# Kernel tuning notes

Hardware: AMD Instinct MI355X
Metric: run time of the kernel (lower is better)

The kernel has to match this reference:

```python
import jax, jax.numpy as jnp
import numpy as np

C = 1.0
SQRT_C = 1.0
EPS = 4e-3        # Poincare ball proj eps for float32
MIN_NORM = 1e-15
N_NODES = 50000
N_EDGES = 800000
NFEAT, NOUT, NHID, HEADS = 128, 64, 32, 4


def _norm(t):
    return jnp.clip(jnp.linalg.norm(t, axis=-1, keepdims=True), MIN_NORM)


def artanh(t):
    t = jnp.clip(t, -1.0 + 1e-7, 1.0 - 1e-7)
    return 0.5 * (jnp.log1p(t) - jnp.log1p(-t))


def proj(t):
    n = _norm(t)
    maxnorm = (1.0 - EPS) / SQRT_C
    return jnp.where(n > maxnorm, t / n * maxnorm, t)


def expmap0(u):
    n = _norm(u)
    return jnp.tanh(SQRT_C * n) * u / (SQRT_C * n)


def logmap0(p):
    n = _norm(p)
    return artanh(SQRT_C * n) * p / (SQRT_C * n)


def mobius_add(a, b):
    a2 = jnp.sum(a * a, -1, keepdims=True)
    b2 = jnp.sum(b * b, -1, keepdims=True)
    ab = jnp.sum(a * b, -1, keepdims=True)
    num = (1.0 + 2.0 * C * ab + C * b2) * a + (1.0 - C * a2) * b
    den = 1.0 + 2.0 * C * ab + C * C * a2 * b2
    return num / jnp.clip(den, MIN_NORM)


def mobius_matvec(W, t):
    mx = t @ W.T
    xn = _norm(t)
    mxn = _norm(mx)
    res = jnp.tanh(mxn / xn * artanh(SQRT_C * xn)) * mx / (mxn * SQRT_C)
    zero = jnp.all(mx == 0, axis=-1, keepdims=True)
    return jnp.where(zero, jnp.zeros_like(res), res)


def hyp_linear(t, W, b):
    res = proj(mobius_matvec(W, t))
    hyp_b = proj(expmap0(b[None, :]))  # proj_tan0 is identity on Poincare ball
    return proj(mobius_add(res, hyp_b))


def leaky_relu(t, slope):
    return jnp.where(t >= 0, t, slope * t)


def hyp_att_agg(h, src, dst, att_i, att_j, heads, concat):
    n = h.shape[0]
    d = h.shape[1] // heads
    ht = logmap0(h)                          # tangent space at origin
    x_i = ht[src].reshape(-1, heads, d)      # target (aggregation) endpoint
    x_j = ht[dst].reshape(-1, heads, d)      # source (message) endpoint
    alpha = (x_i * att_i).sum(-1) + (x_j * att_j).sum(-1)   # [E, heads]
    alpha = leaky_relu(alpha, 0.2)
    amax = jax.ops.segment_max(alpha, src, num_segments=n)
    e = jnp.exp(alpha - amax[src])
    denom = jax.ops.segment_sum(e, src, num_segments=n)
    alpha = e / (denom[src] + 1e-16)
    out = jax.ops.segment_sum(x_j * alpha[..., None], src, num_segments=n)  # [N,h,d]
    out = out.reshape(n, heads * d) if concat else out.mean(axis=1)
    return proj(expmap0(out))


def hyp_act(h, slope=0.01):
    return proj(expmap0(leaky_relu(logmap0(h), slope)))


def _glorot(key, shape):
    fan = shape[-1] + (shape[-2] if len(shape) > 1 else shape[-1])
    a = np.sqrt(6.0 / fan).astype(np.float32)
    return jax.random.uniform(key, shape, jnp.float32, -a, a)


def setup_inputs() -> dict:
    key = jax.random.key(0)
    ks = jax.random.split(key, 12)
    return {
        "x": jax.random.normal(ks[0], (N_NODES, NFEAT), jnp.float32),
        "Wl": _glorot(ks[1], (NOUT, NFEAT)),
        "bl": jnp.zeros((NOUT,), jnp.float32),
        "W1": _glorot(ks[2], (NHID * HEADS, NOUT)),
        "b1": jnp.zeros((NHID * HEADS,), jnp.float32),
        "ai1": _glorot(ks[3], (1, HEADS, NHID)),
        "aj1": _glorot(ks[4], (1, HEADS, NHID)),
        "W2": _glorot(ks[5], (NOUT * HEADS, NHID * HEADS)),
        "b2": jnp.zeros((NOUT * HEADS,), jnp.float32),
        "ai2": _glorot(ks[6], (1, HEADS, NOUT)),
        "aj2": _glorot(ks[7], (1, HEADS, NOUT)),
        "edge_index": jax.random.randint(ks[8], (2, N_EDGES), 0, N_NODES, jnp.int64 if jax.config.jax_enable_x64 else jnp.int32),
    }


def reference(x, Wl, bl, W1, b1, ai1, aj1, W2, b2, ai2, aj2, edge_index):
    n = x.shape[0]
    loops = jnp.arange(n, dtype=edge_index.dtype)
    ei = jnp.concatenate([edge_index, jnp.stack([loops, loops])], axis=1)
    src, dst = ei[0], ei[1]
    h = x @ Wl.T + bl                     # Euclidean linear
    h = proj(expmap0(h))                  # initHyperX (proj_tan0 = identity)
    h = proj(h)
    # layer1: HGATConv(nout -> nhid, heads, concat=True)
    h = hyp_linear(h, W1, b1)
    h = hyp_att_agg(h, src, dst, ai1, aj1, HEADS, True)
    h = hyp_act(h)
    h = proj(h)
    # layer2: HGATConv(nhid*heads -> nout, heads, concat=False)
    h = hyp_linear(h, W2, b2)
    h = hyp_att_agg(h, src, dst, ai2, aj2, HEADS, False)
    h = hyp_act(h)
    return logmap0(h)                     # toTangentX (proj_tan0 = identity)
```

## Files before the change

### kernel.cpp

```cpp
#include <hip/hip_runtime.h>
#include <hip/hip_fp16.h>

#define NN 50000
#define NER 800000
#define NE 850000
#define MAXN 0.996f
#define MINNRM 1e-15f
#define SCAN_B 256
#define NBLK ((NN + SCAN_B - 1) / SCAN_B)
#define HB ((NE + 255) / 256)
#define G0B ((NN + 63) / 64)

typedef _Float16 h2 __attribute__((ext_vector_type(2)));
union UB4 { uint4 u; h2 h[4]; };

__device__ __forceinline__ h2 f2h2(float a, float b){ h2 r; r.x=(_Float16)a; r.y=(_Float16)b; return r; }
__device__ __forceinline__ h2 splat(float a){ h2 r; r.x=(_Float16)a; r.y=(_Float16)a; return r; }

__device__ __forceinline__ float gsum16(float v){
  v += __shfl_xor(v, 1, 64); v += __shfl_xor(v, 2, 64);
  v += __shfl_xor(v, 4, 64); v += __shfl_xor(v, 8, 64);
  return v;
}
__device__ __forceinline__ float gmax16(float v){
  v = fmaxf(v, __shfl_xor(v, 1, 64)); v = fmaxf(v, __shfl_xor(v, 2, 64));
  v = fmaxf(v, __shfl_xor(v, 4, 64)); v = fmaxf(v, __shfl_xor(v, 8, 64));
  return v;
}
__device__ __forceinline__ float artanh_c(float t){
  t = fminf(t, 1.0f - 1e-7f);
  return 0.5f * (log1pf(t) - log1pf(-t));
}
__device__ __forceinline__ float lrelu(float t, float s){ return t >= 0.f ? t : s * t; }

__device__ void bias_blk(const float* b, const float* ai, const float* aj, int L, int HS, float* hbx){
  __shared__ float red[256];
  __shared__ float hai[4], haj[4];
  int t = threadIdx.x;
  float v = (t < L) ? b[t] : 0.f;
  red[t] = v * v; __syncthreads();
  for (int s = 128; s; s >>= 1){ if (t < s) red[t] += red[t + s]; __syncthreads(); }
  float n  = fmaxf(sqrtf(red[0]), MINNRM);
  float un = tanhf(n);
  float nn = un;
  float f  = un / n;
  if (un > MAXN){ f = MAXN / n; nn = MAXN; }
  float hb = v * f;
  if (t < L) hbx[t] = hb;
  if (t < 4){ hai[t] = 0.f; haj[t] = 0.f; }
  __syncthreads();
  if (t < L){
    int h = t / HS;
    atomicAdd(&hai[h], hb * ai[t]);
    atomicAdd(&haj[h], hb * aj[t]);
  }
  __syncthreads();
  if (t == 0) hbx[L] = nn * nn;
  if (t < 4){ hbx[L + 1 + t] = hai[t]; hbx[L + 5 + t] = haj[t]; }
}

__device__ __forceinline__ void wconv(const float* in, __half* outp, int Nr, int Kc, int i){
  int tot = Nr * (Kc >> 1);
  if (i >= tot) return;
  int kp = i / Nr, n = i % Nr;
  __half2 v;
  v.x = __float2half(in[(size_t)n * Kc + 2 * kp]);
  v.y = __float2half(in[(size_t)n * Kc + 2 * kp + 1]);
  ((__half2*)outp)[i] = v;
}

__global__ __launch_bounds__(256) void kprep(
    const float* __restrict__ b1, const float* __restrict__ ai1, const float* __restrict__ aj1, float* __restrict__ hbx1,
    const float* __restrict__ b2, const float* __restrict__ ai2, const float* __restrict__ aj2, float* __restrict__ hbx2,
    const float* __restrict__ Wl, __half* __restrict__ Wlh,
    const float* __restrict__ W1, __half* __restrict__ W1h,
    const float* __restrict__ W2, __half* __restrict__ W2h,
    const int* __restrict__ ei, int* __restrict__ cnt, int* __restrict__ rank){
  int bid = blockIdx.x, tid = threadIdx.x;
  if (bid == 0){ bias_blk(b1, ai1, aj1, 128, 32, hbx1); return; }
  if (bid == 1){ bias_blk(b2, ai2, aj2, 256, 64, hbx2); return; }
  if (bid < 18){ wconv(Wl, Wlh, 64, 128, (bid - 2) * 256 + tid); return; }
  if (bid < 34){ wconv(W1, W1h, 128, 64, (bid - 18) * 256 + tid); return; }
  if (bid < 98){ wconv(W2, W2h, 256, 128, (bid - 34) * 256 + tid); return; }
  int e = (bid - 98) * 256 + tid;
  if (e >= NE) return;
  int s = (e < NER) ? ei[e] : (e - NER);
  rank[e] = atomicAdd(&cnt[s], 1);
}

__device__ void kg0_body(int bid, const float* __restrict__ x, const __half* __restrict__ Wlh,
                         const float* __restrict__ bl, __half* __restrict__ h0h,
                         float* __restrict__ xn0){
  __shared__ __align__(16) h2 As2[16][68];
  __shared__ __align__(16) h2 Bs2[16][68];
  __shared__ float red[64][2];
  int tid = threadIdx.x, wave = tid >> 6, lane = tid & 63;
  int wr = wave >> 1, wc = wave & 1, lr = lane >> 3, lc = lane & 7;
  int row0 = bid * 64;
  int r0 = wr * 32 + lr * 4, c0 = wc * 32 + lc * 4;
  float acc[4][4] = {};
  int am = tid >> 2, aq = tid & 3;
  int bkp = tid >> 4, bn4 = (tid & 15) * 4;
  const uint* Wlu = (const uint*)Wlh;
  float4 ra0, ra1; uint4 rb;
  {
    int row = row0 + am;
    ra0 = make_float4(0.f,0.f,0.f,0.f); ra1 = ra0;
    if (row < NN){
      ra0 = *(const float4*)(x + (size_t)row * 128 + aq * 8);
      ra1 = *(const float4*)(x + (size_t)row * 128 + aq * 8 + 4);
    }
    rb = *(const uint4*)(Wlu + (size_t)bkp * 64 + bn4);
  }
  for (int ks = 0; ks < 4; ks++){
    __syncthreads();
    As2[aq*4+0][am] = f2h2(ra0.x, ra0.y);
    As2[aq*4+1][am] = f2h2(ra0.z, ra0.w);
    As2[aq*4+2][am] = f2h2(ra1.x, ra1.y);
    As2[aq*4+3][am] = f2h2(ra1.z, ra1.w);
    *(uint4*)&Bs2[bkp][bn4] = rb;
    __syncthreads();
    if (ks < 3){
      int k0 = (ks + 1) * 32;
      int row = row0 + am;
      ra0 = make_float4(0.f,0.f,0.f,0.f); ra1 = ra0;
      if (row < NN){
        ra0 = *(const float4*)(x + (size_t)row * 128 + k0 + aq * 8);
        ra1 = *(const float4*)(x + (size_t)row * 128 + k0 + aq * 8 + 4);
      }
      rb = *(const uint4*)(Wlu + (size_t)((ks + 1) * 16 + bkp) * 64 + bn4);
    }
#pragma unroll
    for (int kp = 0; kp < 16; kp++){
      UB4 av, bv;
      av.u = *(const uint4*)&As2[kp][r0];
      bv.u = *(const uint4*)&Bs2[kp][c0];
#pragma unroll
      for (int i = 0; i < 4; i++)
#pragma unroll
        for (int j = 0; j < 4; j++)
          acc[i][j] = __builtin_amdgcn_fdot2(av.h[i], bv.h[j], acc[i][j], false);
    }
  }
  float bb[4];
  *(float4*)&bb[0] = *(const float4*)(bl + c0);
#pragma unroll
  for (int i = 0; i < 4; i++){
    float rs = 0.f;
#pragma unroll
    for (int j = 0; j < 4; j++){ acc[i][j] += bb[j]; rs = fmaf(acc[i][j], acc[i][j], rs); }
    rs += __shfl_xor(rs, 1, 64);
    rs += __shfl_xor(rs, 2, 64);
    rs += __shfl_xor(rs, 4, 64);
    if (lc == 0) red[r0 + i][wc] = rs;
  }
  __syncthreads();
#pragma unroll
  for (int i = 0; i < 4; i++){
    int row = row0 + r0 + i;
    if (row >= NN) continue;
    float rs = red[r0 + i][0] + red[r0 + i][1];
    float n  = fmaxf(sqrtf(rs), MINNRM);
    float un = tanhf(n);
    float f, nm;
    if (un > MAXN){ f = MAXN / n; nm = MAXN; } else { f = un / n; nm = un; }
    union { uint2 u; __half2 h[2]; } st;
    st.h[0] = __floats2half2_rn(acc[i][0] * f, acc[i][1] * f);
    st.h[1] = __floats2half2_rn(acc[i][2] * f, acc[i][3] * f);
    *(uint2*)(h0h + (size_t)row * 64 + c0) = st.u;
    if (wc == 0 && lc == 0) xn0[row] = nm;
  }
}

__global__ __launch_bounds__(256) void kB(const int* __restrict__ cnt,
                                          int* __restrict__ part, int* __restrict__ bsum,
                                          const float* __restrict__ x, const __half* __restrict__ Wlh,
                                          const float* __restrict__ bl, __half* __restrict__ h0h,
                                          float* __restrict__ xn0){
  int bid = blockIdx.x;
  if (bid < NBLK){
    __shared__ int sh[SCAN_B];
    int t = threadIdx.x;
    int i = bid * SCAN_B + t;
    int v = (i < NN) ? cnt[i] : 0;
    sh[t] = v; __syncthreads();
    for (int d = 1; d < SCAN_B; d <<= 1){
      int u = (t >= d) ? sh[t - d] : 0;
      __syncthreads();
      sh[t] += u;
      __syncthreads();
    }
    if (i < NN) part[i] = sh[t];
    if (t == SCAN_B - 1) bsum[bid] = sh[t];
    return;
  }
  kg0_body(bid - NBLK, x, Wlh, bl, h0h, xn0);
}

__global__ __launch_bounds__(256) void kscan2(int* __restrict__ bsum){
  __shared__ int sh[256];
  int t = threadIdx.x;
  int v = (t < NBLK) ? bsum[t] : 0;
  sh[t] = v; __syncthreads();
  for (int d = 1; d < 256; d <<= 1){
    int u = (t >= d) ? sh[t - d] : 0;
    __syncthreads();
    sh[t] += u;
    __syncthreads();
  }
  if (t < NBLK) bsum[t] = sh[t];
}

__global__ __launch_bounds__(SCAN_B) void kscan3(const int* __restrict__ part, const int* __restrict__ bsum,
                                                 const int* __restrict__ cnt, int* __restrict__ rowptr){
  int t = threadIdx.x;
  int i = blockIdx.x * SCAN_B + t;
  if (i < NN){
    int base = blockIdx.x ? bsum[blockIdx.x - 1] : 0;
    rowptr[i] = base + part[i] - cnt[i];
  }
  if (i == 0) rowptr[NN] = bsum[NBLK - 1];
}

__device__ void kg1f_body(int bid, const __half* __restrict__ Ah, const __half* __restrict__ W1h,
    const float* __restrict__ xn0, const float* __restrict__ hbx,
    const float* __restrict__ ai, const float* __restrict__ aj,
    __half* __restrict__ ht1, float* __restrict__ s1i, float* __restrict__ s1j){
  __shared__ __align__(16) h2 As2[16][68];
  __shared__ __align__(16) h2 Bs2[16][132];
  __shared__ float red[64][12];
  int tid = threadIdx.x, wave = tid >> 6, lane = tid & 63;
  int wr = wave >> 1, wc = wave & 1, lr = lane >> 3, lc = lane & 7;
  int row0 = bid * 64;
  int r0 = wr * 32 + lr * 4, c0 = wc * 64 + lc * 8;
  float acc[4][8] = {};
  const uint* Au = (const uint*)Ah;
  const uint* Bu = (const uint*)W1h;
  int akp = tid & 15, am0 = (tid >> 4) * 4;
  int bkp = tid >> 4, bcol = (tid & 15) * 4;
  uint ua0, ua1, ua2, ua3; uint4 ub0, ub1;
  {
    int r;
    ua0 = ua1 = ua2 = ua3 = 0u;
    r = row0 + am0 + 0; if (r < NN) ua0 = Au[(size_t)r * 32 + akp];
    r = row0 + am0 + 1; if (r < NN) ua1 = Au[(size_t)r * 32 + akp];
    r = row0 + am0 + 2; if (r < NN) ua2 = Au[(size_t)r * 32 + akp];
    r = row0 + am0 + 3; if (r < NN) ua3 = Au[(size_t)r * 32 + akp];
    ub0 = *(const uint4*)(Bu + (size_t)bkp * 128 + bcol);
    ub1 = *(const uint4*)(Bu + (size_t)bkp * 128 + bcol + 64);
  }
  for (int ks = 0; ks < 2; ks++){
    __syncthreads();
    { uint4 av4; av4.x = ua0; av4.y = ua1; av4.z = ua2; av4.w = ua3;
      *(uint4*)&As2[akp][am0] = av4; }
    *(uint4*)&Bs2[bkp][bcol]      = ub0;
    *(uint4*)&Bs2[bkp][bcol + 64] = ub1;
    __syncthreads();
    if (ks < 1){
      int r;
      ua0 = ua1 = ua2 = ua3 = 0u;
      r = row0 + am0 + 0; if (r < NN) ua0 = Au[(size_t)r * 32 + 16 + akp];
      r = row0 + am0 + 1; if (r < NN) ua1 = Au[(size_t)r * 32 + 16 + akp];
      r = row0 + am0 + 2; if (r < NN) ua2 = Au[(size_t)r * 32 + 16 + akp];
      r = row0 + am0 + 3; if (r < NN) ua3 = Au[(size_t)r * 32 + 16 + akp];
      ub0 = *(const uint4*)(Bu + (size_t)(16 + bkp) * 128 + bcol);
      ub1 = *(const uint4*)(Bu + (size_t)(16 + bkp) * 128 + bcol + 64);
    }
#pragma unroll
    for (int kp = 0; kp < 16; kp++){
      UB4 av, bv0, bv1;
      av.u  = *(const uint4*)&As2[kp][r0];
      bv0.u = *(const uint4*)&Bs2[kp][c0];
      bv1.u = *(const uint4*)&Bs2[kp][c0 + 4];
#pragma unroll
      for (int i = 0; i < 4; i++){
#pragma unroll
        for (int j = 0; j < 4; j++)
          acc[i][j] = __builtin_amdgcn_fdot2(av.h[i], bv0.h[j], acc[i][j], false);
#pragma unroll
        for (int j = 4; j < 8; j++)
          acc[i][j] = __builtin_amdgcn_fdot2(av.h[i], bv1.h[j - 4], acc[i][j], false);
      }
    }
  }
  float hbv[8], aiv[8], ajv[8];
  *(float4*)&hbv[0] = *(const float4*)(hbx + c0); *(float4*)&hbv[4] = *(const float4*)(hbx + c0 + 4);
  *(float4*)&aiv[0] = *(const float4*)(ai + c0);  *(float4*)&aiv[4] = *(const float4*)(ai + c0 + 4);
  *(float4*)&ajv[0] = *(const float4*)(aj + c0);  *(float4*)&ajv[4] = *(const float4*)(aj + c0 + 4);
  float b2 = hbx[128];
  int head = wc * 2 + (lc >> 2);
#pragma unroll
  for (int i = 0; i < 4; i++){
    float p1=0.f, p2=0.f, pai=0.f, paj=0.f;
#pragma unroll
    for (int j = 0; j < 8; j++){
      float a = acc[i][j];
      p1 += a*a; p2 += a*hbv[j]; pai += a*aiv[j]; paj += a*ajv[j];
    }
    p1 += __shfl_xor(p1,1,64); p1 += __shfl_xor(p1,2,64); p1 += __shfl_xor(p1,4,64);
    p2 += __shfl_xor(p2,1,64); p2 += __shfl_xor(p2,2,64); p2 += __shfl_xor(p2,4,64);
    pai += __shfl_xor(pai,1,64); pai += __shfl_xor(pai,2,64);
    paj += __shfl_xor(paj,1,64); paj += __shfl_xor(paj,2,64);
    int rloc = r0 + i;
    if (lc == 0){ red[rloc][wc] = p1; red[rloc][2+wc] = p2; }
    if ((lc & 3) == 0){ red[rloc][4+head] = pai; red[rloc][8+head] = paj; }
  }
  __syncthreads();
#pragma unroll
  for (int i = 0; i < 4; i++){
    int row = row0 + r0 + i;
    if (row >= NN) continue;
    int rloc = r0 + i;
    float S1 = red[rloc][0] + red[rloc][1];
    float S2 = red[rloc][2] + red[rloc][3];
    float xn = fmaxf(xn0[row], MINNRM);
    float r_art = artanh_c(xn);
    float mxn = fmaxf(sqrtf(S1), MINNRM);
    float tn = tanhf(mxn / xn * r_art);
    float sc_ = tn / mxn;
    float rn = tn;
    if (rn > MAXN){ sc_ *= MAXN / rn; rn = MAXN; }
    float a2r = rn * rn;
    float ab = sc_ * S2;
    float co1 = 1.f + 2.f*ab + b2, co2 = 1.f - a2r;
    float den = fmaxf(1.f + 2.f*ab + a2r*b2, MINNRM);
    float P = co1 * sc_ / den, Q = co2 / den;
    float hn2 = P*P*S1 + 2.f*P*Q*S2 + Q*Q*b2;
    float hn = fmaxf(sqrtf(hn2), MINNRM);
    if (hn > MAXN){ float R = MAXN / hn; P *= R; Q *= R; hn = MAXN; }
    float lf = artanh_c(hn) / hn;
    union { __half h[8]; float4 f4; } ho;
#pragma unroll
    for (int j = 0; j < 8; j++) ho.h[j] = __float2half(lf * (P * acc[i][j] + Q * hbv[j]));
    *(float4*)(ht1 + (size_t)row * 128 + c0) = ho.f4;
    if (lc == 0){
      float pi0 = lf * (P * red[rloc][4+2*wc]   + Q * hbx[129+2*wc]);
      float pi1 = lf * (P * red[rloc][4+2*wc+1] + Q * hbx[129+2*wc+1]);
      float pj0 = lf * (P * red[rloc][8+2*wc]   + Q * hbx[133+2*wc]);
      float pj1 = lf * (P * red[rloc][8+2*wc+1] + Q * hbx[133+2*wc+1]);
      s1i[row*4+2*wc] = pi0; s1i[row*4+2*wc+1] = pi1;
      s1j[row*4+2*wc] = pj0; s1j[row*4+2*wc+1] = pj1;
    }
  }
}

__global__ __launch_bounds__(256) void kE(const int* __restrict__ ei, const int* __restrict__ rowptr,
    const int* __restrict__ rank, int* __restrict__ col,
    const __half* __restrict__ Ah, const __half* __restrict__ W1h,
    const float* __restrict__ xn0, const float* __restrict__ hbx,
    const float* __restrict__ ai, const float* __restrict__ aj,
    __half* __restrict__ ht1, float* __restrict__ s1i, float* __restrict__ s1j){
  int bid = blockIdx.x;
  if (bid >= G0B){
    int e = (bid - G0B) * 256 + threadIdx.x;
    if (e >= NE) return;
    int s, d;
    if (e < NER){ s = ei[e]; d = ei[NER + e]; }
    else { s = e - NER; d = s; }
    col[rowptr[s] + rank[e]] = d;
    return;
  }
  kg1f_body(bid, Ah, W1h, xn0, hbx, ai, aj, ht1, s1i, s1j);
}

__global__ __launch_bounds__(256) void kg2f(const __half* __restrict__ Ah, const __half* __restrict__ W2h,
    const float* __restrict__ xn1, const float* __restrict__ hbx,
    const float* __restrict__ ai, const float* __restrict__ aj,
    __half* __restrict__ ht2, float* __restrict__ s2i, float* __restrict__ s2j){
  __shared__ __align__(16) h2 As2[16][36];
  __shared__ __align__(16) h2 Bs2[16][260];
  __shared__ float red[32][16];
  int tid = threadIdx.x, wave = tid >> 6, lane = tid & 63;
  int wc = wave, lr = lane >> 3, lc = lane & 7;
  int row0 = blockIdx.x * 32;
  int r0 = lr * 4, c0 = wc * 64 + lc * 8;
  float acc[4][8] = {};
  const uint* Au = (const uint*)Ah;
  const uint* Bu = (const uint*)W2h;
  int akp = tid & 15, am0 = (tid >> 4) * 2;
  int brow = tid >> 4, bcol = (tid & 15) * 4;
  uint ua0, ua1;
  uint4 ub0, ub1, ub2, ub3;
  {
    int r;
    ua0 = ua1 = 0u;
    r = row0 + am0 + 0; if (r < NN) ua0 = Au[(size_t)r * 64 + akp];
    r = row0 + am0 + 1; if (r < NN) ua1 = Au[(size_t)r * 64 + akp];
    ub0 = *(const uint4*)(Bu + (size_t)brow * 256 + bcol);
    ub1 = *(const uint4*)(Bu + (size_t)brow * 256 + bcol + 64);
    ub2 = *(const uint4*)(Bu + (size_t)brow * 256 + bcol + 128);
    ub3 = *(const uint4*)(Bu + (size_t)brow * 256 + bcol + 192);
  }
  for (int ks = 0; ks < 4; ks++){
    __syncthreads();
    { uint2 av2; av2.x = ua0; av2.y = ua1;
      *(uint2*)&As2[akp][am0] = av2; }
    *(uint4*)&Bs2[brow][bcol]       = ub0;
    *(uint4*)&Bs2[brow][bcol + 64]  = ub1;
    *(uint4*)&Bs2[brow][bcol + 128] = ub2;
    *(uint4*)&Bs2[brow][bcol + 192] = ub3;
    __syncthreads();
    if (ks < 3){
      int kq = (ks + 1) * 16;
      int r;
      ua0 = ua1 = 0u;
      r = row0 + am0 + 0; if (r < NN) ua0 = Au[(size_t)r * 64 + kq + akp];
      r = row0 + am0 + 1; if (r < NN) ua1 = Au[(size_t)r * 64 + kq + akp];
      ub0 = *(const uint4*)(Bu + (size_t)(kq + brow) * 256 + bcol);
      ub1 = *(const uint4*)(Bu + (size_t)(kq + brow) * 256 + bcol + 64);
      ub2 = *(const uint4*)(Bu + (size_t)(kq + brow) * 256 + bcol + 128);
      ub3 = *(const uint4*)(Bu + (size_t)(kq + brow) * 256 + bcol + 192);
    }
#pragma unroll
    for (int kp = 0; kp < 16; kp++){
      UB4 av, bv0, bv1;
      av.u  = *(const uint4*)&As2[kp][r0];
      bv0.u = *(const uint4*)&Bs2[kp][c0];
      bv1.u = *(const uint4*)&Bs2[kp][c0 + 4];
#pragma unroll
      for (int i = 0; i < 4; i++){
#pragma unroll
        for (int j = 0; j < 4; j++)
          acc[i][j] = __builtin_amdgcn_fdot2(av.h[i], bv0.h[j], acc[i][j], false);
#pragma unroll
        for (int j = 4; j < 8; j++)
          acc[i][j] = __builtin_amdgcn_fdot2(av.h[i], bv1.h[j - 4], acc[i][j], false);
      }
    }
  }
  float hbv[8], aiv[8], ajv[8];
  *(float4*)&hbv[0] = *(const float4*)(hbx + c0); *(float4*)&hbv[4] = *(const float4*)(hbx + c0 + 4);
  *(float4*)&aiv[0] = *(const float4*)(ai + c0);  *(float4*)&aiv[4] = *(const float4*)(ai + c0 + 4);
  *(float4*)&ajv[0] = *(const float4*)(aj + c0);  *(float4*)&ajv[4] = *(const float4*)(aj + c0 + 4);
  float b2 = hbx[256];
#pragma unroll
  for (int i = 0; i < 4; i++){
    float p1=0.f, p2=0.f, pai=0.f, paj=0.f;
#pragma unroll
    for (int j = 0; j < 8; j++){
      float a = acc[i][j];
      p1 += a*a; p2 += a*hbv[j]; pai += a*aiv[j]; paj += a*ajv[j];
    }
    p1 += __shfl_xor(p1,1,64); p1 += __shfl_xor(p1,2,64); p1 += __shfl_xor(p1,4,64);
    p2 += __shfl_xor(p2,1,64); p2 += __shfl_xor(p2,2,64); p2 += __shfl_xor(p2,4,64);
    pai += __shfl_xor(pai,1,64); pai += __shfl_xor(pai,2,64); pai += __shfl_xor(pai,4,64);
    paj += __shfl_xor(paj,1,64); paj += __shfl_xor(paj,2,64); paj += __shfl_xor(paj,4,64);
    int rloc = r0 + i;
    if (lc == 0){ red[rloc][wc] = p1; red[rloc][4+wc] = p2; red[rloc][8+wc] = pai; red[rloc][12+wc] = paj; }
  }
  __syncthreads();
#pragma unroll
  for (int i = 0; i < 4; i++){
    int row = row0 + r0 + i;
    if (row >= NN) continue;
    int rloc = r0 + i;
    float S1 = red[rloc][0]+red[rloc][1]+red[rloc][2]+red[rloc][3];
    float S2 = red[rloc][4]+red[rloc][5]+red[rloc][6]+red[rloc][7];
    float xn = fmaxf(xn1[row], MINNRM);
    float r_art = artanh_c(xn);
    float mxn = fmaxf(sqrtf(S1), MINNRM);
    float tn = tanhf(mxn / xn * r_art);
    float sc_ = tn / mxn;
    float rn = tn;
    if (rn > MAXN){ sc_ *= MAXN / rn; rn = MAXN; }
    float a2r = rn * rn;
    float ab = sc_ * S2;
    float co1 = 1.f + 2.f*ab + b2, co2 = 1.f - a2r;
    float den = fmaxf(1.f + 2.f*ab + a2r*b2, MINNRM);
    float P = co1 * sc_ / den, Q = co2 / den;
    float hn2 = P*P*S1 + 2.f*P*Q*S2 + Q*Q*b2;
    float hn = fmaxf(sqrtf(hn2), MINNRM);
    if (hn > MAXN){ float R = MAXN / hn; P *= R; Q *= R; hn = MAXN; }
    float lf = artanh_c(hn) / hn;
    union { __half h[8]; float4 f4; } ho;
#pragma unroll
    for (int j = 0; j < 8; j++) ho.h[j] = __float2half(lf * (P * acc[i][j] + Q * hbv[j]));
    *(float4*)(ht2 + (size_t)row * 256 + c0) = ho.f4;
    if (lc == 0){
      float pi = lf * (P * red[rloc][8+wc]  + Q * hbx[257+wc]);
      float pj = lf * (P * red[rloc][12+wc] + Q * hbx[261+wc]);
      s2i[row*4+wc] = pi; s2j[row*4+wc] = pj;
    }
  }
}

__global__ __launch_bounds__(256) void k_agg1(const int* __restrict__ rowptr, const int* __restrict__ col,
    const __half* __restrict__ ht1, const float* __restrict__ s1i, const float* __restrict__ s1j,
    __half* __restrict__ hacth, float* __restrict__ xn1){
  __shared__ int    sd[4][4][68];
  __shared__ float4 swl[4][4][66];
  int tid = threadIdx.x, wave = tid >> 6, lane = tid & 63;
  int g = lane >> 4, l = lane & 15, hh = l >> 2;
  int n = blockIdx.x * 16 + wave * 4 + g;
  int p0 = rowptr[n], p1 = rowptr[n + 1];
  float4 si = *(const float4*)(s1i + (size_t)n * 4);
  float m0=-1e30f,m1=-1e30f,m2=-1e30f,m3=-1e30f;
  float s0=0.f,s1=0.f,s2=0.f,s3=0.f;
  h2 acc2[4] = {};
  for (int base = p0; base < p1; base += 64){
    float a[4][4];
#pragma unroll
    for (int ss = 0; ss < 4; ss++){
      a[ss][0] = a[ss][1] = a[ss][2] = a[ss][3] = -1e30f;
      int e = base + ss * 16 + l;
      if (e < p1){
        int d = col[e];
        float4 sj = *(const float4*)(s1j + (size_t)d * 4);
        a[ss][0] = lrelu(si.x + sj.x, 0.2f);
        a[ss][1] = lrelu(si.y + sj.y, 0.2f);
        a[ss][2] = lrelu(si.z + sj.z, 0.2f);
        a[ss][3] = lrelu(si.w + sj.w, 0.2f);
        sd[wave][g][ss * 16 + l] = d;
      }
    }
    float c0 = fmaxf(fmaxf(a[0][0], a[1][0]), fmaxf(a[2][0], a[3][0]));
    float c1 = fmaxf(fmaxf(a[0][1], a[1][1]), fmaxf(a[2][1], a[3][1]));
    float c2 = fmaxf(fmaxf(a[0][2], a[1][2]), fmaxf(a[2][2], a[3][2]));
    float c3 = fmaxf(fmaxf(a[0][3], a[1][3]), fmaxf(a[2][3], a[3][3]));
    float nm0 = fmaxf(m0, gmax16(c0)), nm1 = fmaxf(m1, gmax16(c1));
    float nm2 = fmaxf(m2, gmax16(c2)), nm3 = fmaxf(m3, gmax16(c3));
    float r0_ = __expf(m0 - nm0), r1_ = __expf(m1 - nm1);
    float r2_ = __expf(m2 - nm2), r3_ = __expf(m3 - nm3);
    float t0 = 0.f, t1 = 0.f, t2 = 0.f, t3 = 0.f;
#pragma unroll
    for (int ss = 0; ss < 4; ss++){
      float w0 = __expf(a[ss][0] - nm0), w1 = __expf(a[ss][1] - nm1);
      float w2 = __expf(a[ss][2] - nm2), w3 = __expf(a[ss][3] - nm3);
      swl[wave][g][ss * 16 + l] = make_float4(w0, w1, w2, w3);
      t0 += w0; t1 += w1; t2 += w2; t3 += w3;
    }
    s0 = s0 * r0_ + gsum16(t0); s1 = s1 * r1_ + gsum16(t1);
    s2 = s2 * r2_ + gsum16(t2); s3 = s3 * r3_ + gsum16(t3);
    m0 = nm0; m1 = nm1; m2 = nm2; m3 = nm3;
    float rsel = (hh==0)?r0_:(hh==1)?r1_:(hh==2)?r2_:r3_;
    h2 rs2 = splat(rsel);
#pragma unroll
    for (int j = 0; j < 4; j++) acc2[j] = acc2[j] * rs2;
    __builtin_amdgcn_wave_barrier();
    int cnt_ = min(p1 - base, 64);
    int e = 0;
    for (; e + 3 < cnt_; e += 4){
      int dA = sd[wave][g][e],   dB = sd[wave][g][e+1];
      int dC = sd[wave][g][e+2], dD = sd[wave][g][e+3];
      h2 wA2 = splat(((const float*)&swl[wave][g][e])[hh]);
      h2 wB2 = splat(((const float*)&swl[wave][g][e+1])[hh]);
      h2 wC2 = splat(((const float*)&swl[wave][g][e+2])[hh]);
      h2 wD2 = splat(((const float*)&swl[wave][g][e+3])[hh]);
      UB4 uA, uB, uC, uD;
      uA.u = *(const uint4*)(ht1 + (size_t)dA * 128 + 8*l);
      uB.u = *(const uint4*)(ht1 + (size_t)dB * 128 + 8*l);
      uC.u = *(const uint4*)(ht1 + (size_t)dC * 128 + 8*l);
      uD.u = *(const uint4*)(ht1 + (size_t)dD * 128 + 8*l);
#pragma unroll
      for (int j = 0; j < 4; j++){
        acc2[j] = acc2[j] + wA2 * uA.h[j] + wB2 * uB.h[j] + wC2 * uC.h[j] + wD2 * uD.h[j];
      }
    }
    for (; e < cnt_; e++){
      int dA = sd[wave][g][e];
      h2 wA2 = splat(((const float*)&swl[wave][g][e])[hh]);
      UB4 uA;
      uA.u = *(const uint4*)(ht1 + (size_t)dA * 128 + 8*l);
#pragma unroll
      for (int j = 0; j < 4; j++) acc2[j] = acc2[j] + wA2 * uA.h[j];
    }
    __builtin_amdgcn_wave_barrier();
  }
  float ssel = (hh==0)?s0:(hh==1)?s1:(hh==2)?s2:s3;
  float rinv = 1.f / (ssel + 1e-16f);
  float accf[8];
#pragma unroll
  for (int j = 0; j < 4; j++){ accf[2*j] = (float)acc2[j].x; accf[2*j+1] = (float)acc2[j].y; }
  float sum2 = 0.f;
#pragma unroll
  for (int j = 0; j < 8; j++){ accf[j] *= rinv; sum2 = fmaf(accf[j], accf[j], sum2); }
  sum2 = gsum16(sum2);
  float nn = fmaxf(sqrtf(sum2), MINNRM);
  float un = tanhf(nn);
  float f_, uN;
  if (un > MAXN){ f_ = MAXN / nn; uN = MAXN; } else { f_ = un / nn; uN = un; }
  float lg = artanh_c(uN) / fmaxf(uN, MINNRM);
  float tt[8]; float sum2b = 0.f;
#pragma unroll
  for (int j = 0; j < 8; j++){ tt[j] = lrelu(accf[j] * f_ * lg, 0.01f); sum2b = fmaf(tt[j], tt[j], sum2b); }
  sum2b = gsum16(sum2b);
  float nn2 = fmaxf(sqrtf(sum2b), MINNRM);
  float un2 = tanhf(nn2);
  float f2, nm2v;
  if (un2 > MAXN){ f2 = MAXN / nn2; nm2v = MAXN; } else { f2 = un2 / nn2; nm2v = un2; }
  union { uint4 u; __half2 h[4]; } st;
  st.h[0] = __floats2half2_rn(tt[0]*f2, tt[1]*f2);
  st.h[1] = __floats2half2_rn(tt[2]*f2, tt[3]*f2);
  st.h[2] = __floats2half2_rn(tt[4]*f2, tt[5]*f2);
  st.h[3] = __floats2half2_rn(tt[6]*f2, tt[7]*f2);
  *(uint4*)(hacth + (size_t)n * 128 + 8*l) = st.u;
  if (l == 0) xn1[n] = nm2v;
}

__global__ __launch_bounds__(256) void k_agg2(const int* __restrict__ rowptr, const int* __restrict__ col,
    const __half* __restrict__ ht2, const float* __restrict__ s2i, const float* __restrict__ s2j,
    float* __restrict__ out){
  __shared__ int    sd[4][4][68];
  __shared__ float4 swl[4][4][66];
  int tid = threadIdx.x, wave = tid >> 6, lane = tid & 63;
  int g = lane >> 4, l = lane & 15, hh = l >> 2;
  int n = blockIdx.x * 16 + wave * 4 + g;
  int p0 = rowptr[n], p1 = rowptr[n + 1];
  float4 si = *(const float4*)(s2i + (size_t)n * 4);
  float m0=-1e30f,m1=-1e30f,m2=-1e30f,m3=-1e30f;
  float s0=0.f,s1=0.f,s2=0.f,s3=0.f;
  h2 acc2[8] = {};
  for (int base = p0; base < p1; base += 64){
    float a[4][4];
#pragma unroll
    for (int ss = 0; ss < 4; ss++){
      a[ss][0] = a[ss][1] = a[ss][2] = a[ss][3] = -1e30f;
      int e = base + ss * 16 + l;
      if (e < p1){
        int d = col[e];
        float4 sj = *(const float4*)(s2j + (size_t)d * 4);
        a[ss][0] = lrelu(si.x + sj.x, 0.2f);
        a[ss][1] = lrelu(si.y + sj.y, 0.2f);
        a[ss][2] = lrelu(si.z + sj.z, 0.2f);
        a[ss][3] = lrelu(si.w + sj.w, 0.2f);
        sd[wave][g][ss * 16 + l] = d;
      }
    }
    float c0 = fmaxf(fmaxf(a[0][0], a[1][0]), fmaxf(a[2][0], a[3][0]));
    float c1 = fmaxf(fmaxf(a[0][1], a[1][1]), fmaxf(a[2][1], a[3][1]));
    float c2 = fmaxf(fmaxf(a[0][2], a[1][2]), fmaxf(a[2][2], a[3][2]));
    float c3 = fmaxf(fmaxf(a[0][3], a[1][3]), fmaxf(a[2][3], a[3][3]));
    float nm0 = fmaxf(m0, gmax16(c0)), nm1 = fmaxf(m1, gmax16(c1));
    float nm2 = fmaxf(m2, gmax16(c2)), nm3 = fmaxf(m3, gmax16(c3));
    float r0_ = __expf(m0 - nm0), r1_ = __expf(m1 - nm1);
    float r2_ = __expf(m2 - nm2), r3_ = __expf(m3 - nm3);
    float t0 = 0.f, t1 = 0.f, t2 = 0.f, t3 = 0.f;
#pragma unroll
    for (int ss = 0; ss < 4; ss++){
      float w0 = __expf(a[ss][0] - nm0), w1 = __expf(a[ss][1] - nm1);
      float w2 = __expf(a[ss][2] - nm2), w3 = __expf(a[ss][3] - nm3);
      swl[wave][g][ss * 16 + l] = make_float4(w0, w1, w2, w3);
      t0 += w0; t1 += w1; t2 += w2; t3 += w3;
    }
    s0 = s0 * r0_ + gsum16(t0); s1 = s1 * r1_ + gsum16(t1);
    s2 = s2 * r2_ + gsum16(t2); s3 = s3 * r3_ + gsum16(t3);
    m0 = nm0; m1 = nm1; m2 = nm2; m3 = nm3;
    float rsel = (hh==0)?r0_:(hh==1)?r1_:(hh==2)?r2_:r3_;
    h2 rs2 = splat(rsel);
#pragma unroll
    for (int j = 0; j < 8; j++) acc2[j] = acc2[j] * rs2;
    __builtin_amdgcn_wave_barrier();
    int cnt_ = min(p1 - base, 64);
    int e = 0;
    for (; e + 3 < cnt_; e += 4){
      int dA = sd[wave][g][e],   dB = sd[wave][g][e+1];
      int dC = sd[wave][g][e+2], dD = sd[wave][g][e+3];
      h2 wA2 = splat(((const float*)&swl[wave][g][e])[hh]);
      h2 wB2 = splat(((const float*)&swl[wave][g][e+1])[hh]);
      h2 wC2 = splat(((const float*)&swl[wave][g][e+2])[hh]);
      h2 wD2 = splat(((const float*)&swl[wave][g][e+3])[hh]);
      const __half* pA = ht2 + (size_t)dA * 256 + 16*l;
      const __half* pB = ht2 + (size_t)dB * 256 + 16*l;
      const __half* pC = ht2 + (size_t)dC * 256 + 16*l;
      const __half* pD = ht2 + (size_t)dD * 256 + 16*l;
      UB4 uA0, uA1, uB0, uB1, uC0, uC1, uD0, uD1;
      uA0.u = *(const uint4*)pA; uA1.u = *(const uint4*)(pA + 8);
      uB0.u = *(const uint4*)pB; uB1.u = *(const uint4*)(pB + 8);
      uC0.u = *(const uint4*)pC; uC1.u = *(const uint4*)(pC + 8);
      uD0.u = *(const uint4*)pD; uD1.u = *(const uint4*)(pD + 8);
#pragma unroll
      for (int j = 0; j < 4; j++){
        acc2[j]   = acc2[j]   + wA2 * uA0.h[j] + wB2 * uB0.h[j] + wC2 * uC0.h[j] + wD2 * uD0.h[j];
        acc2[4+j] = acc2[4+j] + wA2 * uA1.h[j] + wB2 * uB1.h[j] + wC2 * uC1.h[j] + wD2 * uD1.h[j];
      }
    }
    for (; e < cnt_; e++){
      int dA = sd[wave][g][e];
      h2 wA2 = splat(((const float*)&swl[wave][g][e])[hh]);
      const __half* pA = ht2 + (size_t)dA * 256 + 16*l;
      UB4 uA0, uA1;
      uA0.u = *(const uint4*)pA; uA1.u = *(const uint4*)(pA + 8);
#pragma unroll
      for (int j = 0; j < 4; j++){
        acc2[j]   = acc2[j]   + wA2 * uA0.h[j];
        acc2[4+j] = acc2[4+j] + wA2 * uA1.h[j];
      }
    }
    __builtin_amdgcn_wave_barrier();
  }
  float ssel = (hh==0)?s0:(hh==1)?s1:(hh==2)?s2:s3;
  float rinv = 1.f / (ssel + 1e-16f);
  float accf[16];
#pragma unroll
  for (int j = 0; j < 4; j++){
    accf[2*j]     = (float)acc2[j].x;   accf[2*j+1]   = (float)acc2[j].y;
    accf[8+2*j]   = (float)acc2[4+j].x; accf[8+2*j+1] = (float)acc2[4+j].y;
  }
  float mj[16]; float sum2 = 0.f;
#pragma unroll
  for (int j = 0; j < 16; j++){
    float v = accf[j] * rinv;
    v += __shfl_xor(v, 4, 64);
    v += __shfl_xor(v, 8, 64);
    mj[j] = 0.25f * v;
    sum2 = fmaf(mj[j], mj[j], sum2);
  }
  sum2 = 0.25f * gsum16(sum2);
  float nn = fmaxf(sqrtf(sum2), MINNRM);
  float un = tanhf(nn);
  float f_, uN;
  if (un > MAXN){ f_ = MAXN / nn; uN = MAXN; } else { f_ = un / nn; uN = un; }
  float lg = artanh_c(uN) / fmaxf(uN, MINNRM);
  float tt[16]; float sum2b = 0.f;
#pragma unroll
  for (int j = 0; j < 16; j++){ tt[j] = lrelu(mj[j] * f_ * lg, 0.01f); sum2b = fmaf(tt[j], tt[j], sum2b); }
  sum2b = 0.25f * gsum16(sum2b);
  float nn2 = fmaxf(sqrtf(sum2b), MINNRM);
  float un2 = tanhf(nn2);
  float f2 = (un2 > MAXN) ? (MAXN / nn2) : (un2 / nn2);
  float uN2 = fminf(un2, MAXN);
  float lg2 = artanh_c(uN2) / fmaxf(uN2, MINNRM);
  if (hh == 0){
    float o[16];
#pragma unroll
    for (int j = 0; j < 16; j++) o[j] = tt[j] * f2 * lg2;
    float* op = out + (size_t)n * 64 + 16*l;
    *(float4*)op      = *(float4*)&o[0];
    *(float4*)(op+4)  = *(float4*)&o[4];
    *(float4*)(op+8)  = *(float4*)&o[8];
    *(float4*)(op+12) = *(float4*)&o[12];
  }
}

extern "C" void kernel_launch(void* const* d_in, const int* in_sizes, int n_in,
                              void* d_out, int out_size, void* d_ws, size_t ws_size,
                              hipStream_t stream){
  const float* x   = (const float*)d_in[0];
  const float* Wl  = (const float*)d_in[1];
  const float* bl  = (const float*)d_in[2];
  const float* W1  = (const float*)d_in[3];
  const float* b1  = (const float*)d_in[4];
  const float* ai1 = (const float*)d_in[5];
  const float* aj1 = (const float*)d_in[6];
  const float* W2  = (const float*)d_in[7];
  const float* b2  = (const float*)d_in[8];
  const float* ai2 = (const float*)d_in[9];
  const float* aj2 = (const float*)d_in[10];
  const int*   ei  = (const int*)d_in[11];
  float* out = (float*)d_out;
  float* ws  = (float*)d_ws;

  __half* h0h   = (__half*)(ws);
  __half* ht1h  = (__half*)(ws + 1600000);
  __half* hacth = (__half*)(ws + 4800000);
  __half* ht2h  = (__half*)(ws + 8000000);
  float* xn0    = ws + 14400000;
  float* xn1    = ws + 14450000;
  float* s1i    = ws + 14500000;
  float* s1j    = ws + 14700000;
  float* hbx1   = ws + 14900000;
  float* hbx2   = ws + 14900144;
  int* rowptr   = (int*)(ws + 14900416);
  int* cnt      = rowptr + NN + 1;
  int* col      = cnt + NN;
  int* part     = col + NE;
  int* bsum     = part + NN;
  int* rank     = bsum + NBLK;
  __half* Wlh   = (__half*)(ws + 16800000);
  __half* W1h   = (__half*)(ws + 16810000);
  __half* W2h   = (__half*)(ws + 16820000);

  hipMemsetAsync(cnt, 0, NN * sizeof(int), stream);
  kprep<<<98 + HB, 256, 0, stream>>>(b1, ai1, aj1, hbx1, b2, ai2, aj2, hbx2,
                                     Wl, Wlh, W1, W1h, W2, W2h, ei, cnt, rank);
  kB<<<NBLK + G0B, 256, 0, stream>>>(cnt, part, bsum, x, Wlh, bl, h0h, xn0);
  kscan2<<<1, 256, 0, stream>>>(bsum);
  kscan3<<<NBLK, SCAN_B, 0, stream>>>(part, bsum, cnt, rowptr);
  kE<<<G0B + HB, 256, 0, stream>>>(ei, rowptr, rank, col, h0h, W1h, xn0, hbx1, ai1, aj1, ht1h, s1i, s1j);
  k_agg1<<<NN / 16, 256, 0, stream>>>(rowptr, col, ht1h, s1i, s1j, hacth, xn1);
  kg2f<<<(NN + 31) / 32, 256, 0, stream>>>(hacth, W2h, xn1, hbx2, ai2, aj2, ht2h, s1i, s1j);
  k_agg2<<<NN / 16, 256, 0, stream>>>(rowptr, col, ht2h, s1i, s1j, out);
}
```

Measured before the change: 268.1 us.

## Use MFMA 16x16x32 f16 for layer-2 hyperbolic linear GEMM

Replaces the LDS-tiled fdot2 GEMM in the layer-2 linear kernel with MFMA matrix-core instructions that load A and B fragments directly from global memory. W2 is now stored row-major in fp16 (a plain conversion) rather than k-pair interleaved, so kprep uses more blocks for it. The epilogue reductions are remapped to the MFMA output layout with 16-lane shuffles, and the output stores become scalar half stores instead of vectorized ones, which may cost some store efficiency.

```diff
diff --git a/kernel.cpp b/kernel.cpp
--- a/kernel.cpp
+++ b/kernel.cpp
@@ -12,6 +12,8 @@
 #define G0B ((NN + 63) / 64)
 
 typedef _Float16 h2 __attribute__((ext_vector_type(2)));
+typedef _Float16 h8 __attribute__((ext_vector_type(8)));
+typedef float f32x4 __attribute__((ext_vector_type(4)));
 union UB4 { uint4 u; h2 h[4]; };
 
 __device__ __forceinline__ h2 f2h2(float a, float b){ h2 r; r.x=(_Float16)a; r.y=(_Float16)b; return r; }
@@ -74,15 +76,19 @@
     const float* __restrict__ b2, const float* __restrict__ ai2, const float* __restrict__ aj2, float* __restrict__ hbx2,
     const float* __restrict__ Wl, __half* __restrict__ Wlh,
     const float* __restrict__ W1, __half* __restrict__ W1h,
-    const float* __restrict__ W2, __half* __restrict__ W2h,
+    const float* __restrict__ W2, __half* __restrict__ W2m,
     const int* __restrict__ ei, int* __restrict__ cnt, int* __restrict__ rank){
   int bid = blockIdx.x, tid = threadIdx.x;
   if (bid == 0){ bias_blk(b1, ai1, aj1, 128, 32, hbx1); return; }
   if (bid == 1){ bias_blk(b2, ai2, aj2, 256, 64, hbx2); return; }
   if (bid < 18){ wconv(Wl, Wlh, 64, 128, (bid - 2) * 256 + tid); return; }
   if (bid < 34){ wconv(W1, W1h, 128, 64, (bid - 18) * 256 + tid); return; }
-  if (bid < 98){ wconv(W2, W2h, 256, 128, (bid - 34) * 256 + tid); return; }
-  int e = (bid - 98) * 256 + tid;
+  if (bid < 162){
+    int i = (bid - 34) * 256 + tid;
+    if (i < 256 * 128) W2m[i] = __float2half(W2[i]);
+    return;
+  }
+  int e = (bid - 162) * 256 + tid;
   if (e >= NE) return;
   int s = (e < NER) ? ei[e] : (e - NER);
   rank[e] = atomicAdd(&cnt[s], 1);
@@ -363,123 +369,116 @@
   kg1f_body(bid, Ah, W1h, xn0, hbx, ai, aj, ht1, s1i, s1j);
 }
 
-__global__ __launch_bounds__(256) void kg2f(const __half* __restrict__ Ah, const __half* __restrict__ W2h,
+__global__ __launch_bounds__(256) void kg2m(const __half* __restrict__ Ah, const __half* __restrict__ W2m,
     const float* __restrict__ xn1, const float* __restrict__ hbx,
     const float* __restrict__ ai, const float* __restrict__ aj,
     __half* __restrict__ ht2, float* __restrict__ s2i, float* __restrict__ s2j){
-  __shared__ __align__(16) h2 As2[16][36];
-  __shared__ __align__(16) h2 Bs2[16][260];
   __shared__ float red[32][16];
-  int tid = threadIdx.x, wave = tid >> 6, lane = tid & 63;
-  int wc = wave, lr = lane >> 3, lc = lane & 7;
+  int tid = threadIdx.x, w = tid >> 6, lane = tid & 63;
+  int lm = lane & 15, lg = lane >> 4;
   int row0 = blockIdx.x * 32;
-  int r0 = lr * 4, c0 = wc * 64 + lc * 8;
-  float acc[4][8] = {};
-  const uint* Au = (const uint*)Ah;
-  const uint* Bu = (const uint*)W2h;
-  int akp = tid & 15, am0 = (tid >> 4) * 2;
-  int brow = tid >> 4, bcol = (tid & 15) * 4;
-  uint ua0, ua1;
-  uint4 ub0, ub1, ub2, ub3;
-  {
-    int r;
-    ua0 = ua1 = 0u;
-    r = row0 + am0 + 0; if (r < NN) ua0 = Au[(size_t)r * 64 + akp];
-    r = row0 + am0 + 1; if (r < NN) ua1 = Au[(size_t)r * 64 + akp];
-    ub0 = *(const uint4*)(Bu + (size_t)brow * 256 + bcol);
-    ub1 = *(const uint4*)(Bu + (size_t)brow * 256 + bcol + 64);
-    ub2 = *(const uint4*)(Bu + (size_t)brow * 256 + bcol + 128);
-    ub3 = *(const uint4*)(Bu + (size_t)brow * 256 + bcol + 192);
-  }
-  for (int ks = 0; ks < 4; ks++){
-    __syncthreads();
-    { uint2 av2; av2.x = ua0; av2.y = ua1;
-      *(uint2*)&As2[akp][am0] = av2; }
-    *(uint4*)&Bs2[brow][bcol]       = ub0;
-    *(uint4*)&Bs2[brow][bcol + 64]  = ub1;
-    *(uint4*)&Bs2[brow][bcol + 128] = ub2;
-    *(uint4*)&Bs2[brow][bcol + 192] = ub3;
-    __syncthreads();
-    if (ks < 3){
-      int kq = (ks + 1) * 16;
-      int r;
-      ua0 = ua1 = 0u;
-      r = row0 + am0 + 0; if (r < NN) ua0 = Au[(size_t)r * 64 + kq + akp];
-      r = row0 + am0 + 1; if (r < NN) ua1 = Au[(size_t)r * 64 + kq + akp];
-      ub0 = *(const uint4*)(Bu + (size_t)(kq + brow) * 256 + bcol);
-      ub1 = *(const uint4*)(Bu + (size_t)(kq + brow) * 256 + bcol + 64);
-      ub2 = *(const uint4*)(Bu + (size_t)(kq + brow) * 256 + bcol + 128);
-      ub3 = *(const uint4*)(Bu + (size_t)(kq + brow) * 256 + bcol + 192);
-    }
-#pragma unroll
-    for (int kp = 0; kp < 16; kp++){
-      UB4 av, bv0, bv1;
-      av.u  = *(const uint4*)&As2[kp][r0];
-      bv0.u = *(const uint4*)&Bs2[kp][c0];
-      bv1.u = *(const uint4*)&Bs2[kp][c0 + 4];
-#pragma unroll
-      for (int i = 0; i < 4; i++){
-#pragma unroll
-        for (int j = 0; j < 4; j++)
-          acc[i][j] = __builtin_amdgcn_fdot2(av.h[i], bv0.h[j], acc[i][j], false);
-#pragma unroll
-        for (int j = 4; j < 8; j++)
-          acc[i][j] = __builtin_amdgcn_fdot2(av.h[i], bv1.h[j - 4], acc[i][j], false);
-      }
-    }
-  }
-  float hbv[8], aiv[8], ajv[8];
-  *(float4*)&hbv[0] = *(const float4*)(hbx + c0); *(float4*)&hbv[4] = *(const float4*)(hbx + c0 + 4);
-  *(float4*)&aiv[0] = *(const float4*)(ai + c0);  *(float4*)&aiv[4] = *(const float4*)(ai + c0 + 4);
-  *(float4*)&ajv[0] = *(const float4*)(aj + c0);  *(float4*)&ajv[4] = *(const float4*)(aj + c0 + 4);
-  float b2 = hbx[256];
-#pragma unroll
-  for (int i = 0; i < 4; i++){
-    float p1=0.f, p2=0.f, pai=0.f, paj=0.f;
-#pragma unroll
-    for (int j = 0; j < 8; j++){
-      float a = acc[i][j];
-      p1 += a*a; p2 += a*hbv[j]; pai += a*aiv[j]; paj += a*ajv[j];
-    }
-    p1 += __shfl_xor(p1,1,64); p1 += __shfl_xor(p1,2,64); p1 += __shfl_xor(p1,4,64);
-    p2 += __shfl_xor(p2,1,64); p2 += __shfl_xor(p2,2,64); p2 += __shfl_xor(p2,4,64);
-    pai += __shfl_xor(pai,1,64); pai += __shfl_xor(pai,2,64); pai += __shfl_xor(pai,4,64);
-    paj += __shfl_xor(paj,1,64); paj += __shfl_xor(paj,2,64); paj += __shfl_xor(paj,4,64);
-    int rloc = r0 + i;
-    if (lc == 0){ red[rloc][wc] = p1; red[rloc][4+wc] = p2; red[rloc][8+wc] = pai; red[rloc][12+wc] = paj; }
+  const _Float16* Af = (const _Float16*)Ah;
+  const _Float16* Bf = (const _Float16*)W2m;
+  const _Float16* A0 = Af + (size_t)(row0 + lm) * 128 + lg * 8;
+  h8 a00 = *(const h8*)(A0);
+  h8 a01 = *(const h8*)(A0 + 32);
+  h8 a02 = *(const h8*)(A0 + 64);
+  h8 a03 = *(const h8*)(A0 + 96);
+  h8 a10, a11, a12, a13;
+  h8 zf = {};
+  bool v1 = (row0 + 31) < NN;
+  if (v1){
+    const _Float16* A1 = Af + (size_t)(row0 + 16 + lm) * 128 + lg * 8;
+    a10 = *(const h8*)(A1);
+    a11 = *(const h8*)(A1 + 32);
+    a12 = *(const h8*)(A1 + 64);
+    a13 = *(const h8*)(A1 + 96);
+  } else { a10 = zf; a11 = zf; a12 = zf; a13 = zf; }
+  f32x4 c00 = {0.f,0.f,0.f,0.f}, c01 = c00, c02 = c00, c03 = c00;
+  f32x4 c10 = c00, c11 = c00, c12 = c00, c13 = c00;
+#define DO_CT(CT, C0, C1) { \
+    const _Float16* Bp = Bf + (size_t)(w * 64 + (CT) * 16 + lm) * 128 + lg * 8; \
+    h8 b0 = *(const h8*)(Bp); \
+    h8 b1 = *(const h8*)(Bp + 32); \
+    h8 b2v = *(const h8*)(Bp + 64); \
+    h8 b3 = *(const h8*)(Bp + 96); \
+    C0 = __builtin_amdgcn_mfma_f32_16x16x32_f16(a00, b0,  C0, 0, 0, 0); \
+    C0 = __builtin_amdgcn_mfma_f32_16x16x32_f16(a01, b1,  C0, 0, 0, 0); \
+    C0 = __builtin_amdgcn_mfma_f32_16x16x32_f16(a02, b2v, C0, 0, 0, 0); \
+    C0 = __builtin_amdgcn_mfma_f32_16x16x32_f16(a03, b3,  C0, 0, 0, 0); \
+    C1 = __builtin_amdgcn_mfma_f32_16x16x32_f16(a10, b0,  C1, 0, 0, 0); \
+    C1 = __builtin_amdgcn_mfma_f32_16x16x32_f16(a11, b1,  C1, 0, 0, 0); \
+    C1 = __builtin_amdgcn_mfma_f32_16x16x32_f16(a12, b2v, C1, 0, 0, 0); \
+    C1 = __builtin_amdgcn_mfma_f32_16x16x32_f16(a13, b3,  C1, 0, 0, 0); }
+  DO_CT(0, c00, c10)
+  DO_CT(1, c01, c11)
+  DO_CT(2, c02, c12)
+  DO_CT(3, c03, c13)
+#undef DO_CT
+  int cb = w * 64 + lm;
+  float hb0 = hbx[cb], hb1 = hbx[cb+16], hb2c = hbx[cb+32], hb3c = hbx[cb+48];
+  float ai0 = ai[cb], ai1v = ai[cb+16], ai2c = ai[cb+32], ai3 = ai[cb+48];
+  float aj0 = aj[cb], aj1v = aj[cb+16], aj2c = aj[cb+32], aj3 = aj[cb+48];
+  float b2s = hbx[256];
+#pragma unroll
+  for (int rt = 0; rt < 2; rt++){
+#pragma unroll
+    for (int ri = 0; ri < 4; ri++){
+      float v0 = rt ? c10[ri] : c00[ri];
+      float v1v = rt ? c11[ri] : c01[ri];
+      float v2v = rt ? c12[ri] : c02[ri];
+      float v3v = rt ? c13[ri] : c03[ri];
+      float p1 = v0*v0 + v1v*v1v + v2v*v2v + v3v*v3v;
+      float p2 = v0*hb0 + v1v*hb1 + v2v*hb2c + v3v*hb3c;
+      float pa = v0*ai0 + v1v*ai1v + v2v*ai2c + v3v*ai3;
+      float pj = v0*aj0 + v1v*aj1v + v2v*aj2c + v3v*aj3;
+      p1 = gsum16(p1); p2 = gsum16(p2); pa = gsum16(pa); pj = gsum16(pj);
+      if (lm == 0){
+        int rloc = rt*16 + lg*4 + ri;
+        red[rloc][w] = p1; red[rloc][4+w] = p2; red[rloc][8+w] = pa; red[rloc][12+w] = pj;
+      }
+    }
   }
   __syncthreads();
 #pragma unroll
-  for (int i = 0; i < 4; i++){
-    int row = row0 + r0 + i;
-    if (row >= NN) continue;
-    int rloc = r0 + i;
-    float S1 = red[rloc][0]+red[rloc][1]+red[rloc][2]+red[rloc][3];
-    float S2 = red[rloc][4]+red[rloc][5]+red[rloc][6]+red[rloc][7];
-    float xn = fmaxf(xn1[row], MINNRM);
-    float r_art = artanh_c(xn);
-    float mxn = fmaxf(sqrtf(S1), MINNRM);
-    float tn = tanhf(mxn / xn * r_art);
-    float sc_ = tn / mxn;
-    float rn = tn;
-    if (rn > MAXN){ sc_ *= MAXN / rn; rn = MAXN; }
-    float a2r = rn * rn;
-    float ab = sc_ * S2;
-    float co1 = 1.f + 2.f*ab + b2, co2 = 1.f - a2r;
-    float den = fmaxf(1.f + 2.f*ab + a2r*b2, MINNRM);
-    float P = co1 * sc_ / den, Q = co2 / den;
-    float hn2 = P*P*S1 + 2.f*P*Q*S2 + Q*Q*b2;
-    float hn = fmaxf(sqrtf(hn2), MINNRM);
-    if (hn > MAXN){ float R = MAXN / hn; P *= R; Q *= R; hn = MAXN; }
-    float lf = artanh_c(hn) / hn;
-    union { __half h[8]; float4 f4; } ho;
-#pragma unroll
-    for (int j = 0; j < 8; j++) ho.h[j] = __float2half(lf * (P * acc[i][j] + Q * hbv[j]));
-    *(float4*)(ht2 + (size_t)row * 256 + c0) = ho.f4;
-    if (lc == 0){
-      float pi = lf * (P * red[rloc][8+wc]  + Q * hbx[257+wc]);
-      float pj = lf * (P * red[rloc][12+wc] + Q * hbx[261+wc]);
-      s2i[row*4+wc] = pi; s2j[row*4+wc] = pj;
+  for (int rt = 0; rt < 2; rt++){
+#pragma unroll
+    for (int ri = 0; ri < 4; ri++){
+      int row = row0 + rt*16 + lg*4 + ri;
+      if (row >= NN) continue;
+      int rloc = rt*16 + lg*4 + ri;
+      float S1 = red[rloc][0]+red[rloc][1]+red[rloc][2]+red[rloc][3];
+      float S2 = red[rloc][4]+red[rloc][5]+red[rloc][6]+red[rloc][7];
+      float xn = fmaxf(xn1[row], MINNRM);
+      float r_art = artanh_c(xn);
+      float mxn = fmaxf(sqrtf(S1), MINNRM);
+      float tn = tanhf(mxn / xn * r_art);
+      float sc_ = tn / mxn;
+      float rn = tn;
+      if (rn > MAXN){ sc_ *= MAXN / rn; rn = MAXN; }
+      float a2r = rn * rn;
+      float ab = sc_ * S2;
+      float co1 = 1.f + 2.f*ab + b2s, co2 = 1.f - a2r;
+      float den = fmaxf(1.f + 2.f*ab + a2r*b2s, MINNRM);
+      float P = co1 * sc_ / den, Q = co2 / den;
+      float hn2 = P*P*S1 + 2.f*P*Q*S2 + Q*Q*b2s;
+      float hn = fmaxf(sqrtf(hn2), MINNRM);
+      if (hn > MAXN){ float R = MAXN / hn; P *= R; Q *= R; hn = MAXN; }
+      float lf = artanh_c(hn) / hn;
+      float v0 = rt ? c10[ri] : c00[ri];
+      float v1v = rt ? c11[ri] : c01[ri];
+      float v2v = rt ? c12[ri] : c02[ri];
+      float v3v = rt ? c13[ri] : c03[ri];
+      __half* hp = ht2 + (size_t)row * 256 + w * 64 + lm;
+      hp[0]  = __float2half(lf * (P * v0  + Q * hb0));
+      hp[16] = __float2half(lf * (P * v1v + Q * hb1));
+      hp[32] = __float2half(lf * (P * v2v + Q * hb2c));
+      hp[48] = __float2half(lf * (P * v3v + Q * hb3c));
+      if (lm == 0){
+        float piv = lf * (P * red[rloc][8+w]  + Q * hbx[257+w]);
+        float pjv = lf * (P * red[rloc][12+w] + Q * hbx[261+w]);
+        s2i[row*4+w] = piv; s2j[row*4+w] = pjv;
+      }
     }
   }
 }
@@ -768,16 +767,16 @@
   int* rank     = bsum + NBLK;
   __half* Wlh   = (__half*)(ws + 16800000);
   __half* W1h   = (__half*)(ws + 16810000);
-  __half* W2h   = (__half*)(ws + 16820000);
+  __half* W2m   = (__half*)(ws + 16820000);
 
   hipMemsetAsync(cnt, 0, NN * sizeof(int), stream);
-  kprep<<<98 + HB, 256, 0, stream>>>(b1, ai1, aj1, hbx1, b2, ai2, aj2, hbx2,
-                                     Wl, Wlh, W1, W1h, W2, W2h, ei, cnt, rank);
+  kprep<<<162 + HB, 256, 0, stream>>>(b1, ai1, aj1, hbx1, b2, ai2, aj2, hbx2,
+                                      Wl, Wlh, W1, W1h, W2, W2m, ei, cnt, rank);
   kB<<<NBLK + G0B, 256, 0, stream>>>(cnt, part, bsum, x, Wlh, bl, h0h, xn0);
   kscan2<<<1, 256, 0, stream>>>(bsum);
   kscan3<<<NBLK, SCAN_B, 0, stream>>>(part, bsum, cnt, rowptr);
   kE<<<G0B + HB, 256, 0, stream>>>(ei, rowptr, rank, col, h0h, W1h, xn0, hbx1, ai1, aj1, ht1h, s1i, s1j);
   k_agg1<<<NN / 16, 256, 0, stream>>>(rowptr, col, ht1h, s1i, s1j, hacth, xn1);
-  kg2f<<<(NN + 31) / 32, 256, 0, stream>>>(hacth, W2h, xn1, hbx2, ai2, aj2, ht2h, s1i, s1j);
+  kg2m<<<(NN + 31) / 32, 256, 0, stream>>>(hacth, W2m, xn1, hbx2, ai2, aj2, ht2h, s1i, s1j);
   k_agg2<<<NN / 16, 256, 0, stream>>>(rowptr, col, ht2h, s1i, s1j, out);
 }
```

Result: slower. 275.9 us (+2.9%).
